# Optimization experiments

Measured on AMD Instinct MI355X. Metric: run time of the kernel, lower is better.

Reference implementation:

```python
import jax, jax.numpy as jnp
import numpy as np

N_CLASSES = 10
N_INTERNAL = 256
ELEMS_PER_NODE = 3


def build_circuit(seed=0):
    """Deterministic SDD-like DAG in topological order.
    Node ids: 0..9 = positive class literals, 10..19 = negated literals,
    20.. = internal decision nodes. Each decision node is a list of
    (prime_id, sub_id) element pairs; primes are distinct positive literals
    (mutually-exclusive events) so node values stay bounded in [0,1]."""
    rng = np.random.RandomState(seed)
    n_base = 2 * N_CLASSES
    nodes = []
    for i in range(N_INTERNAL):
        avail = n_base + i
        primes = rng.choice(N_CLASSES, size=ELEMS_PER_NODE, replace=False)
        subs = rng.randint(0, avail, size=ELEMS_PER_NODE)
        nodes.append([(int(p), int(s)) for p, s in zip(primes, subs)])
    return nodes

CIRCUIT = build_circuit(0)


def eval_sdd(probs):
    # probs: [B, 10] softmax outputs. WMC semiring: (add, mul, 0, 1).
    vals = [probs[:, v] for v in range(N_CLASSES)]
    vals += [1.0 - probs[:, v] for v in range(N_CLASSES)]
    for elems in CIRCUIT:
        acc = vals[elems[0][0]] * vals[elems[0][1]]
        for p, s in elems[1:]:
            acc = acc + vals[p] * vals[s]
        vals.append(acc)
    return vals[-1]  # root node, shape [B]


def setup_inputs() -> dict:
    key = jax.random.key(0)
    ks = jax.random.split(key, 7)
    B, D_IN, H, C = 8192, 784, 4096, N_CLASSES
    s1 = 1.0 / np.sqrt(D_IN)
    s2 = 1.0 / np.sqrt(H)
    return {
        "x": jax.random.normal(ks[0], (B, D_IN), dtype=jnp.float32),
        "W1": jax.random.uniform(ks[1], (D_IN, H), jnp.float32, -s1, s1),
        "b1": jnp.zeros((H,), jnp.float32),
        "W2": jax.random.uniform(ks[2], (H, H), jnp.float32, -s2, s2),
        "b2": jnp.zeros((H,), jnp.float32),
        "W3": jax.random.uniform(ks[3], (H, C), jnp.float32, -s2, s2),
        "b3": jnp.zeros((C,), jnp.float32),
    }


def reference(x, W1, b1, W2, b2, W3, b3):
    h = jax.nn.relu(x @ W1 + b1)          # [B, H]
    h = jax.nn.relu(h @ W2 + b2)          # [B, H]
    logits = h @ W3 + b3                  # [B, 10]
    probs = jax.nn.softmax(logits, axis=-1)
    return eval_sdd(probs)                # [B]
```

## Files before the change

kernel.cpp:

```cpp
#include <hip/hip_runtime.h>
#include <cstdint>
#include <cstddef>

constexpr int N_CLASSES  = 10;
constexpr int N_INTERNAL = 256;
constexpr int N_VALS     = 2 * N_CLASSES + N_INTERNAL;
constexpr int B_SZ  = 8192;
constexpr int D_IN  = 784;
constexpr int KP1   = 896;
constexpr int H_DIM = 4096;

struct MTState {
  uint32_t key[624];
  int pos;
};

constexpr uint32_t mt_next(MTState& st) {
  if (st.pos == 624) {
    for (int i = 0; i < 624; ++i) {
      uint32_t y = (st.key[i] & 0x80000000u) | (st.key[(i + 1) % 624] & 0x7fffffffu);
      st.key[i] = st.key[(i + 397) % 624] ^ (y >> 1) ^ ((y & 1u) ? 0x9908b0dfu : 0u);
    }
    st.pos = 0;
  }
  uint32_t y = st.key[st.pos++];
  y ^= y >> 11;
  y ^= (y << 7) & 0x9d2c5680u;
  y ^= (y << 15) & 0xefc60000u;
  y ^= y >> 18;
  return y;
}

constexpr uint32_t interval_draw(MTState& st, uint32_t maxv) {
  if (maxv == 0u) return 0u;
  uint32_t mask = maxv;
  mask |= mask >> 1; mask |= mask >> 2; mask |= mask >> 4;
  mask |= mask >> 8; mask |= mask >> 16;
  uint32_t v = mt_next(st) & mask;
  while (v > maxv) v = mt_next(st) & mask;
  return v;
}

struct Circuit {
  int16_t prime[N_INTERNAL][3];
  int16_t sub[N_INTERNAL][3];
};

constexpr Circuit make_circuit() {
  MTState st{};
  uint32_t s = 0u;
  for (int i = 0; i < 624; ++i) {
    st.key[i] = s;
    s = 1812433253u * (s ^ (s >> 30)) + (uint32_t)i + 1u;
  }
  st.pos = 624;

  Circuit c{};
  for (int node = 0; node < N_INTERNAL; ++node) {
    const int avail = 2 * N_CLASSES + node;
    int arr[N_CLASSES] = {0, 1, 2, 3, 4, 5, 6, 7, 8, 9};
    for (int i = N_CLASSES - 1; i >= 1; --i) {
      uint32_t j = interval_draw(st, (uint32_t)i);
      int tmp = arr[i]; arr[i] = arr[j]; arr[j] = tmp;
    }
    for (int e = 0; e < 3; ++e) c.prime[node][e] = (int16_t)arr[e];
    for (int e = 0; e < 3; ++e) c.sub[node][e] = (int16_t)interval_draw(st, (uint32_t)(avail - 1));
  }
  return c;
}

constexpr Circuit CIRC = make_circuit();

__device__ __forceinline__ uint16_t f2bf(float f) {
  uint32_t u = __builtin_bit_cast(uint32_t, f);
  uint32_t r = (u + 0x7fffu + ((u >> 16) & 1u)) >> 16;
  return (uint16_t)r;
}
__device__ __forceinline__ float bf2f(uint16_t h) {
  uint32_t u = ((uint32_t)h) << 16;
  return __builtin_bit_cast(float, u);
}

__device__ __forceinline__ void load_lds16(const void* g, void* l) {
  __builtin_amdgcn_global_load_lds(
      (const __attribute__((address_space(1))) unsigned int*)g,
      (__attribute__((address_space(3))) unsigned int*)l, 16, 0, 0);
}

using bf16x8 = __attribute__((ext_vector_type(8))) short;
using f32x4  = __attribute__((ext_vector_type(4))) float;
using u16x8  = __attribute__((ext_vector_type(8))) unsigned short;
using u16x4  = __attribute__((ext_vector_type(4))) unsigned short;

template <int IMM>
__device__ __forceinline__ void dsr_i(bf16x8& d, uint32_t a) {
  asm volatile("ds_read_b128 %0, %1 offset:%2" : "=v"(d) : "v"(a), "n"(IMM));
}

template <int I>
__device__ __forceinline__ void eval_node(float (&vals)[N_VALS]) {
  if constexpr (I < N_INTERNAL) {
    constexpr int p0 = CIRC.prime[I][0], s0 = CIRC.sub[I][0];
    constexpr int p1 = CIRC.prime[I][1], s1 = CIRC.sub[I][1];
    constexpr int p2 = CIRC.prime[I][2], s2 = CIRC.sub[I][2];
    vals[2 * N_CLASSES + I] =
        vals[p0] * vals[s0] + vals[p1] * vals[s1] + vals[p2] * vals[s2];
    eval_node<I + 1>(vals);
  }
}

__device__ __forceinline__ void transpose_tile64(
    const float* __restrict__ W, uint16_t* __restrict__ Wt,
    int K, int N, int Kp, int kt, int nt, int t) {
  __shared__ float tile[64][65];
  const int lr = t >> 4;
  const int lc = (t & 15) * 4;
#pragma unroll
  for (int p = 0; p < 4; ++p) {
    const int row = lr + p * 16;
    const int k = kt + row;
    float4 v = {0.f, 0.f, 0.f, 0.f};
    if (k < K) v = *reinterpret_cast<const float4*>(W + (size_t)k * N + nt + lc);
    tile[row][lc + 0] = v.x;
    tile[row][lc + 1] = v.y;
    tile[row][lc + 2] = v.z;
    tile[row][lc + 3] = v.w;
  }
  __syncthreads();
  const int wn = t >> 3;
  const int k8 = (t & 7) * 8;
#pragma unroll
  for (int p = 0; p < 2; ++p) {
    const int n = nt + wn + 32 * p;
    u16x8 o;
#pragma unroll
    for (int i = 0; i < 8; ++i) o[i] = f2bf(tile[k8 + i][wn + 32 * p]);
    *reinterpret_cast<u16x8*>(Wt + (size_t)n * Kp + kt + k8) = o;
  }
}

__global__ __launch_bounds__(256) void prep_kernel(
    const float* __restrict__ x, const float* __restrict__ W1,
    const float* __restrict__ W2, uint16_t* __restrict__ xb,
    uint16_t* __restrict__ w1t, uint16_t* __restrict__ w2t) {
  const int b = blockIdx.x;
  const int t = threadIdx.x;
  if (b < B_SZ) {
    if (t < D_IN / 4) {
      float4 v = *reinterpret_cast<const float4*>(x + (size_t)b * D_IN + t * 4);
      u16x4 o;
      o[0] = f2bf(v.x); o[1] = f2bf(v.y); o[2] = f2bf(v.z); o[3] = f2bf(v.w);
      *reinterpret_cast<u16x4*>(xb + (size_t)b * KP1 + t * 4) = o;
    } else if (t < KP1 / 4) {
      u16x4 z = {0, 0, 0, 0};
      *reinterpret_cast<u16x4*>(xb + (size_t)b * KP1 + t * 4) = z;
    }
  } else if (b < B_SZ + (KP1 / 64) * (H_DIM / 64)) {
    const int tt = b - B_SZ;
    const int nt = (tt & 63) * 64;
    const int kt = (tt >> 6) * 64;
    transpose_tile64(W1, w1t, D_IN, H_DIM, KP1, kt, nt, t);
  } else {
    const int tt = b - B_SZ - (KP1 / 64) * (H_DIM / 64);
    const int nt = (tt & 63) * 64;
    const int kt = (tt >> 6) * 64;
    transpose_tile64(W2, w2t, H_DIM, H_DIM, H_DIM, kt, nt, t);
  }
}

template <int MH, int NH, int BUF, bool RA, bool RB, int VM, typename F>
__device__ __forceinline__ void phase_t(
    uint32_t aA0, uint32_t aA1, uint32_t bA0, uint32_t bA1,
    bf16x8 (&Ar)[4][2], bf16x8 (&Br)[2][2][2], f32x4 (&acc)[2][2][4][2],
    F&& stage) {
  constexpr int AO = BUF * 32768 + MH * 16384;
  constexpr int BO = BUF * 32768 + NH * 16384;
  if constexpr (RA) {
    dsr_i<AO + 0 * 2048>(Ar[0][0], aA0); dsr_i<AO + 0 * 2048>(Ar[0][1], aA1);
    dsr_i<AO + 1 * 2048>(Ar[1][0], aA0); dsr_i<AO + 1 * 2048>(Ar[1][1], aA1);
    dsr_i<AO + 2 * 2048>(Ar[2][0], aA0); dsr_i<AO + 2 * 2048>(Ar[2][1], aA1);
    dsr_i<AO + 3 * 2048>(Ar[3][0], aA0); dsr_i<AO + 3 * 2048>(Ar[3][1], aA1);
  }
  if constexpr (RB) {
    dsr_i<BO + 0 * 2048>(Br[NH][0][0], bA0); dsr_i<BO + 0 * 2048>(Br[NH][0][1], bA1);
    dsr_i<BO + 1 * 2048>(Br[NH][1][0], bA0); dsr_i<BO + 1 * 2048>(Br[NH][1][1], bA1);
  }
  stage();
  asm volatile("s_waitcnt lgkmcnt(0)" ::: "memory");
  __builtin_amdgcn_sched_barrier(0);
  __builtin_amdgcn_s_setprio(1);
#pragma unroll
  for (int m = 0; m < 4; ++m)
#pragma unroll
    for (int nf = 0; nf < 2; ++nf) {
      acc[MH][NH][m][nf] = __builtin_amdgcn_mfma_f32_16x16x32_bf16(
          Ar[m][0], Br[NH][nf][0], acc[MH][NH][m][nf], 0, 0, 0);
      acc[MH][NH][m][nf] = __builtin_amdgcn_mfma_f32_16x16x32_bf16(
          Ar[m][1], Br[NH][nf][1], acc[MH][NH][m][nf], 0, 0, 0);
    }
  __builtin_amdgcn_s_setprio(0);
  if constexpr (VM >= 0) asm volatile("s_waitcnt vmcnt(%0)" :: "i"(VM) : "memory");
  __builtin_amdgcn_s_barrier();
}

__global__ __launch_bounds__(512, 1) void gemm256_bf16(
    const uint16_t* __restrict__ A, const uint16_t* __restrict__ Bt,
    const float* __restrict__ bias, uint16_t* __restrict__ C,
    int M, int N, int K) {
  extern __shared__ char smem[];

  const int t    = threadIdx.x;
  const int t16  = t * 16;
  const int lane = t & 63;
  const int wid  = t >> 6;
  const int wr   = wid >> 2;
  const int wc   = wid & 3;
  const int fr   = lane & 15;
  const int fq   = lane >> 4;

  const int gx = gridDim.x, gy = gridDim.y;
  const int nwg = gx * gy;
  const int id  = blockIdx.y * gx + blockIdx.x;
  const int cpx = nwg >> 3;
  const int sid = (id & 7) * cpx + (id >> 3);
  const int row0 = (sid / gx) * 256;
  const int col0 = (sid % gx) * 256;

  const uint32_t Kb = (uint32_t)K * 2;

  const char* gA = (const char*)A + (size_t)row0 * Kb;
  const char* gB = (const char*)Bt + (size_t)col0 * Kb;

  const uint32_t prow = (uint32_t)(t >> 3);
  const uint32_t sg   = (uint32_t)(((t & 7) ^ (t >> 3)) & 7) * 16u;
  const uint32_t srcA = prow * Kb + sg;
  const uint32_t srcB = (prow + 32u * (prow >> 5)) * Kb + sg;

#define ROWA(h, j) ((h) * 64 + (j) * 128)
#define ROWB(h, j) ((h) * 32 + (j) * 128)

#define STAGE_A(v, h, kt) do { \
    load_lds16(gA + (size_t)(kt) * 128 + (size_t)ROWA(h, 0) * Kb + srcA, \
               smem + (v) * 32768 + (h) * 16384 + t16); \
    load_lds16(gA + (size_t)(kt) * 128 + (size_t)ROWA(h, 1) * Kb + srcA, \
               smem + (v) * 32768 + (h) * 16384 + 8192 + t16); } while (0)
#define STAGE_B(v, h, kt) do { \
    load_lds16(gB + (size_t)(kt) * 128 + (size_t)ROWB(h, 0) * Kb + srcB, \
               smem + 65536 + (v) * 32768 + (h) * 16384 + t16); \
    load_lds16(gB + (size_t)(kt) * 128 + (size_t)ROWB(h, 1) * Kb + srcB, \
               smem + 65536 + (v) * 32768 + (h) * 16384 + 8192 + t16); } while (0)

  const uint32_t smb = (uint32_t)(size_t)(__attribute__((address_space(3))) char*)smem;
  const uint32_t s0v = (uint32_t)(((fq) ^ (fr & 7)) * 16);
  const uint32_t aA0 = smb + (uint32_t)((wr * 64 + fr) * 128) + s0v;
  const uint32_t aA1 = smb + (uint32_t)((wr * 64 + fr) * 128) + (s0v ^ 64u);
  const uint32_t bA0 = smb + 65536u + (uint32_t)((wc * 32 + fr) * 128) + s0v;
  const uint32_t bA1 = smb + 65536u + (uint32_t)((wc * 32 + fr) * 128) + (s0v ^ 64u);

  f32x4 acc[2][2][4][2];
#pragma unroll
  for (int a = 0; a < 2; ++a)
#pragma unroll
    for (int b = 0; b < 2; ++b)
#pragma unroll
      for (int m = 0; m < 4; ++m)
#pragma unroll
        for (int n = 0; n < 2; ++n) {
          acc[a][b][m][n][0] = 0.f; acc[a][b][m][n][1] = 0.f;
          acc[a][b][m][n][2] = 0.f; acc[a][b][m][n][3] = 0.f;
        }

  bf16x8 Ar[4][2], Br[2][2][2];

  STAGE_A(0, 0, 0); STAGE_B(0, 0, 0); STAGE_A(0, 1, 0); STAGE_B(0, 1, 0);
  STAGE_A(1, 0, 1); STAGE_B(1, 1, 1); STAGE_A(1, 1, 1);
  asm volatile("s_waitcnt vmcnt(6)" ::: "memory");
  __builtin_amdgcn_s_barrier();

#define PH(MH_, NH_, RA_, RB_, VM_, BUF_, ...) \
  phase_t<MH_, NH_, BUF_, RA_, RB_, VM_>(aA0, aA1, bA0, bA1, \
                                         Ar, Br, acc, [&]() { __VA_ARGS__ })

  const int NI = K >> 7;
  int i = 0;
  for (; i < NI - 1; ++i) {
    const int ktb = 2 * i + 1, ktc = 2 * i + 2, ktd = 2 * i + 3;
    PH(0, 0, true,  true,  -1, 0, STAGE_B(1, 0, ktb); );
    PH(0, 1, false, true,  -1, 0, STAGE_A(0, 0, ktc); );
    PH(1, 1, true,  false, -1, 0, STAGE_B(0, 1, ktc); );
    PH(1, 0, false, true,   6, 0, STAGE_A(0, 1, ktc); );
    PH(0, 0, true,  true,  -1, 1, STAGE_B(0, 0, ktc); );
    PH(0, 1, false, true,  -1, 1, STAGE_A(1, 0, ktd); );
    PH(1, 1, true,  false, -1, 1, STAGE_B(1, 1, ktd); );
    PH(1, 0, false, true,   6, 1, STAGE_A(1, 1, ktd); );
  }
  {
    const int ktb = 2 * i + 1;
    PH(0, 0, true,  true,  -1, 0, STAGE_B(1, 0, ktb); );
    PH(0, 1, false, true,  -1, 0, );
    PH(1, 1, true,  false, -1, 0, );
    PH(1, 0, false, true,   0, 0, );
    PH(0, 0, true,  true,  -1, 1, );
    PH(0, 1, false, true,  -1, 1, );
    PH(1, 1, true,  false, -1, 1, );
    PH(1, 0, false, true,  -1, 1, );
  }
#undef PH
#undef STAGE_A
#undef STAGE_B
#undef ROWA
#undef ROWB

#pragma unroll
  for (int mh = 0; mh < 2; ++mh)
#pragma unroll
    for (int nh = 0; nh < 2; ++nh)
#pragma unroll
      for (int m = 0; m < 4; ++m)
#pragma unroll
        for (int nf = 0; nf < 2; ++nf) {
          const int row = row0 + wr * 128 + mh * 64 + m * 16 + fq * 4;
          const int col = col0 + wc * 64 + nh * 32 + nf * 16 + fr;
          const float bv = bias[col];
          const size_t base = (size_t)row * N + col;
#pragma unroll
          for (int j = 0; j < 4; ++j) {
            float v = acc[mh][nh][m][nf][j] + bv;
            v = fmaxf(v, 0.0f);
            C[base + (size_t)j * N] = f2bf(v);
          }
        }
}

__global__ __launch_bounds__(256) void logits_circuit_kernel(
    const uint16_t* __restrict__ h2, const float* __restrict__ W3,
    const float* __restrict__ b3, float* __restrict__ out, int B) {
  const int wave = threadIdx.x >> 6;
  const int lane = threadIdx.x & 63;
  const int row  = blockIdx.x * 4 + wave;
  if (row >= B) return;

  const uint16_t* hrow = h2 + (size_t)row * H_DIM;
  float acc[N_CLASSES];
#pragma unroll
  for (int c = 0; c < N_CLASSES; ++c) acc[c] = 0.0f;

#pragma unroll
  for (int it = 0; it < H_DIM / (64 * 8); ++it) {
    const int k0 = (it * 64 + lane) * 8;
    ushort4 u0 = *reinterpret_cast<const ushort4*>(hrow + k0);
    ushort4 u1 = *reinterpret_cast<const ushort4*>(hrow + k0 + 4);
    float hv[8] = {bf2f(u0.x), bf2f(u0.y), bf2f(u0.z), bf2f(u0.w),
                   bf2f(u1.x), bf2f(u1.y), bf2f(u1.z), bf2f(u1.w)};
#pragma unroll
    for (int q = 0; q < 8; ++q) {
      const float* wrow = W3 + (size_t)(k0 + q) * N_CLASSES;
#pragma unroll
      for (int c = 0; c < N_CLASSES; ++c) acc[c] = fmaf(hv[q], wrow[c], acc[c]);
    }
  }

#pragma unroll
  for (int c = 0; c < N_CLASSES; ++c) {
#pragma unroll
    for (int s = 32; s >= 1; s >>= 1) acc[c] += __shfl_xor(acc[c], s, 64);
  }

  float l[N_CLASSES], m = -3.0e38f;
#pragma unroll
  for (int c = 0; c < N_CLASSES; ++c) {
    l[c] = acc[c] + b3[c];
    m = fmaxf(m, l[c]);
  }
  float sum = 0.0f;
#pragma unroll
  for (int c = 0; c < N_CLASSES; ++c) {
    l[c] = expf(l[c] - m);
    sum += l[c];
  }
  const float inv = 1.0f / sum;

  float vals[N_VALS];
#pragma unroll
  for (int c = 0; c < N_CLASSES; ++c) {
    const float p = l[c] * inv;
    vals[c] = p;
    vals[N_CLASSES + c] = 1.0f - p;
  }
  eval_node<0>(vals);
  if (lane == 0) out[row] = vals[N_VALS - 1];
}

extern "C" void kernel_launch(void* const* d_in, const int* in_sizes, int n_in,
                              void* d_out, int out_size, void* d_ws, size_t ws_size,
                              hipStream_t stream) {
  const float* x  = (const float*)d_in[0];
  const float* W1 = (const float*)d_in[1];
  const float* b1 = (const float*)d_in[2];
  const float* W2 = (const float*)d_in[3];
  const float* b2 = (const float*)d_in[4];
  const float* W3 = (const float*)d_in[5];
  const float* b3 = (const float*)d_in[6];
  float* out = (float*)d_out;

  uint16_t* xb  = (uint16_t*)d_ws;
  uint16_t* w1t = xb  + (size_t)B_SZ * KP1;
  uint16_t* w2t = w1t + (size_t)H_DIM * KP1;
  uint16_t* h1  = w2t + (size_t)H_DIM * H_DIM;
  uint16_t* h2  = h1  + (size_t)B_SZ * H_DIM;

  (void)hipFuncSetAttribute((const void*)gemm256_bf16,
                            hipFuncAttributeMaxDynamicSharedMemorySize, 131072);

  dim3 blk(256);

  const int prep_blocks = B_SZ + (KP1 / 64) * (H_DIM / 64) + (H_DIM / 64) * (H_DIM / 64);
  prep_kernel<<<dim3(prep_blocks), blk, 0, stream>>>(x, W1, W2, xb, w1t, w2t);

  gemm256_bf16<<<dim3(H_DIM / 256, B_SZ / 256), dim3(512), 131072, stream>>>(
      xb, w1t, b1, h1, B_SZ, H_DIM, KP1);

  gemm256_bf16<<<dim3(H_DIM / 256, B_SZ / 256), dim3(512), 131072, stream>>>(
      h1, w2t, b2, h2, B_SZ, H_DIM, H_DIM);

  logits_circuit_kernel<<<dim3(B_SZ / 4), blk, 0, stream>>>(h2, W3, b3, out, B_SZ);
}
```

Baseline: 404.7 us.

## Split GEMM LDS reads into halves overlapping MFMA; transpose W3 for vector loads

The GEMM phase now issues the global-stage copy first, then reads A/B fragments from LDS in two K-halves. It waits only on the first half before running its MFMAs, so the second-half LDS reads overlap compute. Separately, W3 is transposed to class-major layout inside the prep kernel, which lets the logits kernel load float4 weight vectors instead of scalar strided loads. This costs an extra small transpose and some workspace, and relies on the lgkmcnt counting of outstanding LDS reads being correct.

New measurement: 353.0 us. -12.8%, faster.

```diff
diff --git a/kernel.cpp b/kernel.cpp
--- a/kernel.cpp
+++ b/kernel.cpp
@@ -141,10 +141,13 @@
 
 __global__ __launch_bounds__(256) void prep_kernel(
     const float* __restrict__ x, const float* __restrict__ W1,
-    const float* __restrict__ W2, uint16_t* __restrict__ xb,
-    uint16_t* __restrict__ w1t, uint16_t* __restrict__ w2t) {
+    const float* __restrict__ W2, const float* __restrict__ W3,
+    uint16_t* __restrict__ xb, uint16_t* __restrict__ w1t,
+    uint16_t* __restrict__ w2t, float* __restrict__ w3t) {
   const int b = blockIdx.x;
   const int t = threadIdx.x;
+  constexpr int W1_T = (KP1 / 64) * (H_DIM / 64);
+  constexpr int W2_T = (H_DIM / 64) * (H_DIM / 64);
   if (b < B_SZ) {
     if (t < D_IN / 4) {
       float4 v = *reinterpret_cast<const float4*>(x + (size_t)b * D_IN + t * 4);
@@ -155,16 +158,17 @@
       u16x4 z = {0, 0, 0, 0};
       *reinterpret_cast<u16x4*>(xb + (size_t)b * KP1 + t * 4) = z;
     }
-  } else if (b < B_SZ + (KP1 / 64) * (H_DIM / 64)) {
+  } else if (b < B_SZ + W1_T) {
     const int tt = b - B_SZ;
-    const int nt = (tt & 63) * 64;
-    const int kt = (tt >> 6) * 64;
-    transpose_tile64(W1, w1t, D_IN, H_DIM, KP1, kt, nt, t);
+    transpose_tile64(W1, w1t, D_IN, H_DIM, KP1, (tt >> 6) * 64, (tt & 63) * 64, t);
+  } else if (b < B_SZ + W1_T + W2_T) {
+    const int tt = b - B_SZ - W1_T;
+    transpose_tile64(W2, w2t, H_DIM, H_DIM, H_DIM, (tt >> 6) * 64, (tt & 63) * 64, t);
   } else {
-    const int tt = b - B_SZ - (KP1 / 64) * (H_DIM / 64);
-    const int nt = (tt & 63) * 64;
-    const int kt = (tt >> 6) * 64;
-    transpose_tile64(W2, w2t, H_DIM, H_DIM, H_DIM, kt, nt, t);
+    const int row = (b - B_SZ - W1_T - W2_T) * 256 + t;
+#pragma unroll
+    for (int c = 0; c < N_CLASSES; ++c)
+      w3t[(size_t)c * H_DIM + row] = W3[(size_t)row * N_CLASSES + c];
   }
 }
 
@@ -175,29 +179,45 @@
     F&& stage) {
   constexpr int AO = BUF * 32768 + MH * 16384;
   constexpr int BO = BUF * 32768 + NH * 16384;
+  stage();
   if constexpr (RA) {
-    dsr_i<AO + 0 * 2048>(Ar[0][0], aA0); dsr_i<AO + 0 * 2048>(Ar[0][1], aA1);
-    dsr_i<AO + 1 * 2048>(Ar[1][0], aA0); dsr_i<AO + 1 * 2048>(Ar[1][1], aA1);
-    dsr_i<AO + 2 * 2048>(Ar[2][0], aA0); dsr_i<AO + 2 * 2048>(Ar[2][1], aA1);
-    dsr_i<AO + 3 * 2048>(Ar[3][0], aA0); dsr_i<AO + 3 * 2048>(Ar[3][1], aA1);
+    dsr_i<AO + 0 * 2048>(Ar[0][0], aA0);
+    dsr_i<AO + 1 * 2048>(Ar[1][0], aA0);
+    dsr_i<AO + 2 * 2048>(Ar[2][0], aA0);
+    dsr_i<AO + 3 * 2048>(Ar[3][0], aA0);
   }
   if constexpr (RB) {
-    dsr_i<BO + 0 * 2048>(Br[NH][0][0], bA0); dsr_i<BO + 0 * 2048>(Br[NH][0][1], bA1);
-    dsr_i<BO + 1 * 2048>(Br[NH][1][0], bA0); dsr_i<BO + 1 * 2048>(Br[NH][1][1], bA1);
-  }
-  stage();
+    dsr_i<BO + 0 * 2048>(Br[NH][0][0], bA0);
+    dsr_i<BO + 1 * 2048>(Br[NH][1][0], bA0);
+  }
+  if constexpr (RA) {
+    dsr_i<AO + 0 * 2048>(Ar[0][1], aA1);
+    dsr_i<AO + 1 * 2048>(Ar[1][1], aA1);
+    dsr_i<AO + 2 * 2048>(Ar[2][1], aA1);
+    dsr_i<AO + 3 * 2048>(Ar[3][1], aA1);
+  }
+  if constexpr (RB) {
+    dsr_i<BO + 0 * 2048>(Br[NH][0][1], bA1);
+    dsr_i<BO + 1 * 2048>(Br[NH][1][1], bA1);
+  }
+  constexpr int S1 = (RA ? 4 : 0) + (RB ? 2 : 0);
+  asm volatile("s_waitcnt lgkmcnt(%0)" :: "i"(S1) : "memory");
+  __builtin_amdgcn_sched_barrier(0);
+  __builtin_amdgcn_s_setprio(1);
+#pragma unroll
+  for (int m = 0; m < 4; ++m)
+#pragma unroll
+    for (int nf = 0; nf < 2; ++nf)
+      acc[MH][NH][m][nf] = __builtin_amdgcn_mfma_f32_16x16x32_bf16(
+          Ar[m][0], Br[NH][nf][0], acc[MH][NH][m][nf], 0, 0, 0);
   asm volatile("s_waitcnt lgkmcnt(0)" ::: "memory");
   __builtin_amdgcn_sched_barrier(0);
-  __builtin_amdgcn_s_setprio(1);
 #pragma unroll
   for (int m = 0; m < 4; ++m)
 #pragma unroll
-    for (int nf = 0; nf < 2; ++nf) {
-      acc[MH][NH][m][nf] = __builtin_amdgcn_mfma_f32_16x16x32_bf16(
-          Ar[m][0], Br[NH][nf][0], acc[MH][NH][m][nf], 0, 0, 0);
+    for (int nf = 0; nf < 2; ++nf)
       acc[MH][NH][m][nf] = __builtin_amdgcn_mfma_f32_16x16x32_bf16(
           Ar[m][1], Br[NH][nf][1], acc[MH][NH][m][nf], 0, 0, 0);
-    }
   __builtin_amdgcn_s_setprio(0);
   if constexpr (VM >= 0) asm volatile("s_waitcnt vmcnt(%0)" :: "i"(VM) : "memory");
   __builtin_amdgcn_s_barrier();
@@ -333,7 +353,7 @@
 }
 
 __global__ __launch_bounds__(256) void logits_circuit_kernel(
-    const uint16_t* __restrict__ h2, const float* __restrict__ W3,
+    const uint16_t* __restrict__ h2, const float* __restrict__ w3t,
     const float* __restrict__ b3, float* __restrict__ out, int B) {
   const int wave = threadIdx.x >> 6;
   const int lane = threadIdx.x & 63;
@@ -350,13 +370,19 @@
     const int k0 = (it * 64 + lane) * 8;
     ushort4 u0 = *reinterpret_cast<const ushort4*>(hrow + k0);
     ushort4 u1 = *reinterpret_cast<const ushort4*>(hrow + k0 + 4);
-    float hv[8] = {bf2f(u0.x), bf2f(u0.y), bf2f(u0.z), bf2f(u0.w),
-                   bf2f(u1.x), bf2f(u1.y), bf2f(u1.z), bf2f(u1.w)};
-#pragma unroll
-    for (int q = 0; q < 8; ++q) {
-      const float* wrow = W3 + (size_t)(k0 + q) * N_CLASSES;
-#pragma unroll
-      for (int c = 0; c < N_CLASSES; ++c) acc[c] = fmaf(hv[q], wrow[c], acc[c]);
+    const float hv[8] = {bf2f(u0.x), bf2f(u0.y), bf2f(u0.z), bf2f(u0.w),
+                         bf2f(u1.x), bf2f(u1.y), bf2f(u1.z), bf2f(u1.w)};
+#pragma unroll
+    for (int c = 0; c < N_CLASSES; ++c) {
+      const float* wr = w3t + (size_t)c * H_DIM + k0;
+      float4 w0 = *reinterpret_cast<const float4*>(wr);
+      float4 w1 = *reinterpret_cast<const float4*>(wr + 4);
+      float a = acc[c];
+      a = fmaf(hv[0], w0.x, a); a = fmaf(hv[1], w0.y, a);
+      a = fmaf(hv[2], w0.z, a); a = fmaf(hv[3], w0.w, a);
+      a = fmaf(hv[4], w1.x, a); a = fmaf(hv[5], w1.y, a);
+      a = fmaf(hv[6], w1.z, a); a = fmaf(hv[7], w1.w, a);
+      acc[c] = a;
     }
   }
 
@@ -408,14 +434,16 @@
   uint16_t* w2t = w1t + (size_t)H_DIM * KP1;
   uint16_t* h1  = w2t + (size_t)H_DIM * H_DIM;
   uint16_t* h2  = h1  + (size_t)B_SZ * H_DIM;
+  float* w3t    = (float*)(h2 + (size_t)B_SZ * H_DIM);
 
   (void)hipFuncSetAttribute((const void*)gemm256_bf16,
                             hipFuncAttributeMaxDynamicSharedMemorySize, 131072);
 
   dim3 blk(256);
 
-  const int prep_blocks = B_SZ + (KP1 / 64) * (H_DIM / 64) + (H_DIM / 64) * (H_DIM / 64);
-  prep_kernel<<<dim3(prep_blocks), blk, 0, stream>>>(x, W1, W2, xb, w1t, w2t);
+  const int prep_blocks =
+      B_SZ + (KP1 / 64) * (H_DIM / 64) + (H_DIM / 64) * (H_DIM / 64) + H_DIM / 256;
+  prep_kernel<<<dim3(prep_blocks), blk, 0, stream>>>(x, W1, W2, W3, xb, w1t, w2t, w3t);
 
   gemm256_bf16<<<dim3(H_DIM / 256, B_SZ / 256), dim3(512), 131072, stream>>>(
       xb, w1t, b1, h1, B_SZ, H_DIM, KP1);
@@ -423,5 +451,5 @@
   gemm256_bf16<<<dim3(H_DIM / 256, B_SZ / 256), dim3(512), 131072, stream>>>(
       h1, w2t, b2, h2, B_SZ, H_DIM, H_DIM);
 
-  logits_circuit_kernel<<<dim3(B_SZ / 4), blk, 0, stream>>>(h2, W3, b3, out, B_SZ);
-}
+  logits_circuit_kernel<<<dim3(B_SZ / 4), blk, 0, stream>>>(h2, w3t, b3, out, B_SZ);
+}
```
